# Kernel optimization log

Measured on AMD Instinct MI355X. Metric: run time of the kernel, lower is better.

The kernel has to match this reference:

```python
import jax, jax.numpy as jnp
import numpy as np

N_NODES = 100000


def _add_self_loops(edge_index, n):
    loop = jnp.arange(n, dtype=edge_index.dtype)
    src = jnp.concatenate([edge_index[0], loop])
    dst = jnp.concatenate([edge_index[1], loop])
    return src, dst


def _gcn_conv(x, W, b, src, dst, n):
    # h = X W, then symmetric-normalized scatter-add over edges (PyG GCNConv)
    h = x @ W
    ones = jnp.ones(src.shape[0], dtype=h.dtype)
    deg = jax.ops.segment_sum(ones, dst, num_segments=n)  # in-degree incl. self loops
    dinv = jnp.where(deg > 0, jax.lax.rsqrt(deg), 0.0)
    norm = dinv[src] * dinv[dst]                           # [E]
    msg = h[src] * norm[:, None]                           # gather + scale
    out = jax.ops.segment_sum(msg, dst, num_segments=n)    # scatter-add
    return out + b


def setup_inputs() -> dict:
    key = jax.random.key(0)
    k1, k2, k3, k4 = jax.random.split(key, 4)
    F, H, C = 128, 128, 16
    x = jax.random.normal(k1, (N_NODES, F), dtype=jnp.float32)
    edge_index = jax.random.randint(k2, (2, 1600000), 0, N_NODES, dtype=jnp.int64)
    W1 = jax.random.normal(k3, (F, H), dtype=jnp.float32) / np.sqrt(F)
    b1 = jnp.zeros((H,), dtype=jnp.float32)
    W2 = jax.random.normal(k4, (H, C), dtype=jnp.float32) / np.sqrt(H)
    b2 = jnp.zeros((C,), dtype=jnp.float32)
    return {"x": x, "edge_index": edge_index, "W1": W1, "b1": b1, "W2": W2, "b2": b2}


def reference(x, edge_index, W1, b1, W2, b2):
    n = x.shape[0]
    src, dst = _add_self_loops(edge_index, n)
    h = _gcn_conv(x, W1, b1, src, dst, n)
    h = jax.nn.relu(h)
    # dropout(p=0.1) treated as identity (deterministic eval-mode reference)
    logits = _gcn_conv(h, W2, b2, src, dst, n)
    return logits, jax.nn.log_softmax(logits, axis=1)
```

## Files before the change

kernel.cpp:

```cpp
#include <hip/hip_runtime.h>
#include <math.h>


#define ELLW 72
#define EPB 16384
#define BSH 9
#define MAXEB 100
#define MAXBK 200

typedef __attribute__((ext_vector_type(8))) short short8;
typedef __attribute__((ext_vector_type(4))) float f32x4;
typedef __attribute__((ext_vector_type(4))) int i32x4;
typedef __attribute__((ext_vector_type(4))) _Float16 f16x4;

__device__ __forceinline__ float bf2f(unsigned short u) {
    return __uint_as_float(((unsigned int)u) << 16);
}
__device__ __forceinline__ unsigned short f2bf(float f) {
    unsigned int u = __float_as_uint(f);
    unsigned int r = (u + 0x7fffu + ((u >> 16) & 1u)) >> 16;
    return (unsigned short)r;
}
__device__ __forceinline__ f32x4 h2f4(f16x4 v) {
    f32x4 r;
    r[0] = (float)v[0]; r[1] = (float)v[1]; r[2] = (float)v[2]; r[3] = (float)v[3];
    return r;
}

__global__ void k_prep_hist(unsigned short* __restrict__ h, _Float16* __restrict__ g,
                            const float* __restrict__ W1, unsigned short* __restrict__ wt,
                            int n, const int* __restrict__ dst, int E,
                            int* __restrict__ hist, int nbuck, float* __restrict__ dinv) {
    __shared__ int lh[MAXBK];
    const int t = threadIdx.x;
    if (blockIdx.x < 64) {
        int i = blockIdx.x * 256 + t;
        if (i < 16384) {
            int nc = i >> 7, k = i & 127;
            wt[i] = f2bf(W1[k * 128 + nc]);
        }
        if (i < 128) h[(size_t)n * 128 + i] = 0;
        if (i < 16) g[(size_t)n * 16 + i] = (_Float16)0.f;
        if (i < 1) dinv[n] = 1.f;
        return;
    }
    const int blk = blockIdx.x - 64;
    for (int i = t; i < nbuck; i += 256) lh[i] = 0;
    __syncthreads();
    const int e0 = blk * EPB;
    const int e1 = min(e0 + EPB, E);
    for (int e = e0 + t; e < e1; e += 256)
        atomicAdd(&lh[dst[e] >> BSH], 1);
    __syncthreads();
    for (int i = t; i < nbuck; i += 256)
        hist[blk * nbuck + i] = lh[i];
}

__global__ void k_scan(int* __restrict__ hist, int* __restrict__ bstart,
                       int* __restrict__ bcount, int neb, int nbuck) {
    __shared__ unsigned short lh[MAXEB * MAXBK];
    __shared__ int sc[256];
    const int t = threadIdx.x;
    const int items = neb * nbuck;
    const int it4 = items >> 2;
    for (int i = t; i < it4; i += 256) {
        i32x4 v = *(const i32x4*)(hist + i * 4);
        lh[i * 4 + 0] = (unsigned short)v[0];
        lh[i * 4 + 1] = (unsigned short)v[1];
        lh[i * 4 + 2] = (unsigned short)v[2];
        lh[i * 4 + 3] = (unsigned short)v[3];
    }
    for (int i = (it4 << 2) + t; i < items; i += 256)
        lh[i] = (unsigned short)hist[i];
    __syncthreads();
    int total = 0;
    if (t < nbuck)
        for (int blk = 0; blk < neb; ++blk) total += lh[blk * nbuck + t];
    sc[t] = total;
    __syncthreads();
    for (int o = 1; o < 256; o <<= 1) {
        int x = 0;
        if (t >= o) x = sc[t - o];
        __syncthreads();
        if (t >= o) sc[t] += x;
        __syncthreads();
    }
    if (t < nbuck) {
        int run = sc[t] - total;
        bstart[t] = run;
        bcount[t] = total;
        for (int blk = 0; blk < neb; ++blk) {
            int idx = blk * nbuck + t;
            int v = lh[idx];
            hist[idx] = run;
            run += v;
        }
    }
}

__global__ __launch_bounds__(256) void k_bin_gemm(
        const int* __restrict__ src, const int* __restrict__ dst, int E,
        const int* __restrict__ hist, int* __restrict__ binned, int nbuck, int neb,
        const float* __restrict__ x, const unsigned short* __restrict__ wt,
        unsigned short* __restrict__ h, int n) {
    __shared__ unsigned short xs[64 * 136];
    const int t = threadIdx.x;
    if ((int)blockIdx.x < neb) {
        int* cnt = (int*)xs;
        const int blk = blockIdx.x;
        for (int i = t; i < nbuck; i += 256) cnt[i] = hist[blk * nbuck + i];
        __syncthreads();
        const int e0 = blk * EPB;
        const int e1 = min(e0 + EPB, E);
        for (int e = e0 + t; e < e1; e += 256) {
            int d = dst[e];
            int b = d >> BSH;
            int pos = atomicAdd(&cnt[b], 1);
            binned[pos] = src[e] | ((d & ((1 << BSH) - 1)) << 17);
        }
        return;
    }
    const int row0 = ((int)blockIdx.x - neb) * 64;
    for (int i = t; i < 2048; i += 256) {
        int r = i >> 5, c4 = (i & 31) << 2;
        int gr = row0 + r;
        float4 v = make_float4(0.f, 0.f, 0.f, 0.f);
        if (gr < n) v = *(const float4*)(x + (size_t)gr * 128 + c4);
        ushort4 u;
        u.x = f2bf(v.x); u.y = f2bf(v.y); u.z = f2bf(v.z); u.w = f2bf(v.w);
        *(ushort4*)(xs + r * 136 + c4) = u;
    }
    __syncthreads();
    const int w = t >> 6;
    const int lane = t & 63;
    const int m = lane & 15, q = lane >> 4;
    f32x4 acc[8];
#pragma unroll
    for (int ns = 0; ns < 8; ++ns) acc[ns] = (f32x4){0.f, 0.f, 0.f, 0.f};
#pragma unroll
    for (int kt = 0; kt < 4; ++kt) {
        short8 a = *(const short8*)(xs + (w * 16 + m) * 136 + kt * 32 + q * 8);
#pragma unroll
        for (int ns = 0; ns < 8; ++ns) {
            short8 b = *(const short8*)((const short*)wt + (ns * 16 + m) * 128 + kt * 32 + q * 8);
            acc[ns] = __builtin_amdgcn_mfma_f32_16x16x32_bf16(a, b, acc[ns], 0, 0, 0);
        }
    }
    unsigned short* xsw = xs + (w * 16) * 136;
#pragma unroll
    for (int ns = 0; ns < 8; ++ns)
#pragma unroll
        for (int reg = 0; reg < 4; ++reg)
            xsw[(q * 4 + reg) * 136 + ns * 16 + m] = f2bf(acc[ns][reg]);
    __syncthreads();
#pragma unroll
    for (int it = 0; it < 8; ++it) {
        int rl = (lane >> 5) + it * 2;
        int off = (lane & 31) * 4;
        int gr = row0 + w * 16 + rl;
        if (gr < n)
            *(ushort4*)(h + (size_t)gr * 128 + off) = *(const ushort4*)(xsw + rl * 136 + off);
    }
}

__global__ void k_ell(const int* __restrict__ binned, const int* __restrict__ bstart,
                      const int* __restrict__ bcount, int* __restrict__ deg,
                      float* __restrict__ dinv, int* __restrict__ col, int n) {
    __shared__ int ldeg[1 << BSH];
    const int t = threadIdx.x, b = blockIdx.x;
    const int node0 = b << BSH;
    for (int i = t; i < (1 << BSH); i += 256) ldeg[i] = 0;
    __syncthreads();
    const int st = bstart[b], cv = bcount[b];
    for (int i = t; i < cv; i += 256) {
        int v = binned[st + i];
        int s = v & 0x1FFFF;
        int dl = v >> 17;
        int q = atomicAdd(&ldeg[dl], 1);
        if (q < ELLW) col[(size_t)(node0 + dl) * ELLW + q] = s;
    }
    __syncthreads();
    for (int i = t; i < (1 << BSH); i += 256) {
        int node = node0 + i;
        if (node < n) {
            int dgv = ldeg[i];
            deg[node] = dgv;
            int dc = dgv > ELLW ? ELLW : dgv;
            dinv[node] = rsqrtf((float)(dc + 1));
            int kend = (dc + 7) & ~7;
            for (int q = dc; q < kend; ++q) col[(size_t)node * ELLW + q] = n;
        }
    }
}

__global__ __launch_bounds__(256, 2) void k_gather1f(
        const unsigned short* __restrict__ h, const int* __restrict__ deg,
        const float* __restrict__ dinv, const int* __restrict__ col,
        const float* __restrict__ b1, const float* __restrict__ W2,
        _Float16* __restrict__ g, int n) {
    const int t = threadIdx.x;
    const int lane = t & 15;
    const int d = blockIdx.x * 16 + (t >> 4);
    if (d >= n) return;
    int dg = deg[d];
    if (dg > ELLW) dg = ELLW;
    const float dd = dinv[d];
    const int kend = (dg + 7) & ~7;
    const int* ecol = col + (size_t)d * ELLW;

    float aA[8], aB[8];
    {
        short8 u = *(const short8*)(h + (size_t)d * 128 + lane * 8);
#pragma unroll
        for (int j = 0; j < 8; ++j) {
            aA[j] = dd * bf2f((unsigned short)u[j]);
            aB[j] = 0.f;
        }
    }
    for (int k = 0; k < kend; k += 8) {
        int4 c0 = *(const int4*)(ecol + k);
        int4 c1 = *(const int4*)(ecol + k + 4);
        float e0 = dinv[c0.x], e1 = dinv[c0.y], e2 = dinv[c0.z], e3 = dinv[c0.w];
        float e4 = dinv[c1.x], e5 = dinv[c1.y], e6 = dinv[c1.z], e7 = dinv[c1.w];
        short8 u0 = *(const short8*)(h + (size_t)c0.x * 128 + lane * 8);
        short8 u1 = *(const short8*)(h + (size_t)c0.y * 128 + lane * 8);
        short8 u2 = *(const short8*)(h + (size_t)c0.z * 128 + lane * 8);
        short8 u3 = *(const short8*)(h + (size_t)c0.w * 128 + lane * 8);
        short8 u4 = *(const short8*)(h + (size_t)c1.x * 128 + lane * 8);
        short8 u5 = *(const short8*)(h + (size_t)c1.y * 128 + lane * 8);
        short8 u6 = *(const short8*)(h + (size_t)c1.z * 128 + lane * 8);
        short8 u7 = *(const short8*)(h + (size_t)c1.w * 128 + lane * 8);
#pragma unroll
        for (int j = 0; j < 8; ++j) {
            aA[j] = fmaf(bf2f((unsigned short)u0[j]), e0, aA[j]);
            aB[j] = fmaf(bf2f((unsigned short)u1[j]), e1, aB[j]);
            aA[j] = fmaf(bf2f((unsigned short)u2[j]), e2, aA[j]);
            aB[j] = fmaf(bf2f((unsigned short)u3[j]), e3, aB[j]);
            aA[j] = fmaf(bf2f((unsigned short)u4[j]), e4, aA[j]);
            aB[j] = fmaf(bf2f((unsigned short)u5[j]), e5, aB[j]);
            aA[j] = fmaf(bf2f((unsigned short)u6[j]), e6, aA[j]);
            aB[j] = fmaf(bf2f((unsigned short)u7[j]), e7, aB[j]);
        }
    }
    float y[8];
    const float* b1p = b1 + lane * 8;
#pragma unroll
    for (int j = 0; j < 8; ++j)
        y[j] = fmaxf(fmaf(aA[j] + aB[j], dd, b1p[j]), 0.f);
    const float4* w2v = (const float4*)(W2 + lane * 8 * 16);
    float4 z0 = make_float4(0.f, 0.f, 0.f, 0.f);
    float4 z1 = z0, z2 = z0, z3 = z0;
#pragma unroll
    for (int j = 0; j < 8; ++j) {
        float4 w0 = w2v[j * 4 + 0], w1 = w2v[j * 4 + 1];
        float4 w2 = w2v[j * 4 + 2], w3 = w2v[j * 4 + 3];
        float yj = y[j];
        z0.x = fmaf(yj, w0.x, z0.x); z0.y = fmaf(yj, w0.y, z0.y);
        z0.z = fmaf(yj, w0.z, z0.z); z0.w = fmaf(yj, w0.w, z0.w);
        z1.x = fmaf(yj, w1.x, z1.x); z1.y = fmaf(yj, w1.y, z1.y);
        z1.z = fmaf(yj, w1.z, z1.z); z1.w = fmaf(yj, w1.w, z1.w);
        z2.x = fmaf(yj, w2.x, z2.x); z2.y = fmaf(yj, w2.y, z2.y);
        z2.z = fmaf(yj, w2.z, z2.z); z2.w = fmaf(yj, w2.w, z2.w);
        z3.x = fmaf(yj, w3.x, z3.x); z3.y = fmaf(yj, w3.y, z3.y);
        z3.z = fmaf(yj, w3.z, z3.z); z3.w = fmaf(yj, w3.w, z3.w);
    }
#pragma unroll
    for (int mm = 1; mm < 16; mm <<= 1) {
        z0.x += __shfl_xor(z0.x, mm); z0.y += __shfl_xor(z0.y, mm);
        z0.z += __shfl_xor(z0.z, mm); z0.w += __shfl_xor(z0.w, mm);
        z1.x += __shfl_xor(z1.x, mm); z1.y += __shfl_xor(z1.y, mm);
        z1.z += __shfl_xor(z1.z, mm); z1.w += __shfl_xor(z1.w, mm);
        z2.x += __shfl_xor(z2.x, mm); z2.y += __shfl_xor(z2.y, mm);
        z2.z += __shfl_xor(z2.z, mm); z2.w += __shfl_xor(z2.w, mm);
        z3.x += __shfl_xor(z3.x, mm); z3.y += __shfl_xor(z3.y, mm);
        z3.z += __shfl_xor(z3.z, mm); z3.w += __shfl_xor(z3.w, mm);
    }
    if (lane < 4) {
        float4 z = (lane == 0) ? z0 : (lane == 1) ? z1 : (lane == 2) ? z2 : z3;
        f16x4 zz;
        zz[0] = (_Float16)(z.x * dd); zz[1] = (_Float16)(z.y * dd);
        zz[2] = (_Float16)(z.z * dd); zz[3] = (_Float16)(z.w * dd);
        *(f16x4*)(g + (size_t)d * 16 + lane * 4) = zz;
    }
}

__global__ void k_gather2(const _Float16* __restrict__ g, const int* __restrict__ deg,
                          const int* __restrict__ col, const float* __restrict__ b2,
                          float* __restrict__ out, int n) {
    const int t = threadIdx.x;
    const int d = blockIdx.x * 64 + (t >> 2);
    if (d >= n) return;
    const int l = t & 3;
    int dg = deg[d];
    if (dg > ELLW) dg = ELLW;
    const float dd = rsqrtf((float)(dg + 1));
    const int kend = (dg + 7) & ~7;
    const int* ecol = col + (size_t)d * ELLW;
    const _Float16* gl = g + l * 4;

    f32x4 aA = h2f4(*(const f16x4*)(gl + (size_t)d * 16));
    f32x4 aB = (f32x4){0.f, 0.f, 0.f, 0.f};
    f32x4 aC = aB, aD = aB;
    for (int k = 0; k < kend; k += 8) {
        int4 c0 = *(const int4*)(ecol + k);
        int4 c1 = *(const int4*)(ecol + k + 4);
        f16x4 h0 = *(const f16x4*)(gl + (size_t)c0.x * 16);
        f16x4 h1 = *(const f16x4*)(gl + (size_t)c0.y * 16);
        f16x4 h2 = *(const f16x4*)(gl + (size_t)c0.z * 16);
        f16x4 h3 = *(const f16x4*)(gl + (size_t)c0.w * 16);
        f16x4 h4 = *(const f16x4*)(gl + (size_t)c1.x * 16);
        f16x4 h5 = *(const f16x4*)(gl + (size_t)c1.y * 16);
        f16x4 h6 = *(const f16x4*)(gl + (size_t)c1.z * 16);
        f16x4 h7 = *(const f16x4*)(gl + (size_t)c1.w * 16);
        aA += h2f4(h0); aB += h2f4(h1); aC += h2f4(h2); aD += h2f4(h3);
        aA += h2f4(h4); aB += h2f4(h5); aC += h2f4(h6); aD += h2f4(h7);
    }
    f32x4 bv = *(const f32x4*)(b2 + l * 4);
    f32x4 acc = (aA + aB + aC + aD) * dd + bv;
    *(f32x4*)(out + (size_t)d * 16 + l * 4) = acc;
    float m = fmaxf(fmaxf(acc[0], acc[1]), fmaxf(acc[2], acc[3]));
    m = fmaxf(m, __shfl_xor(m, 1));
    m = fmaxf(m, __shfl_xor(m, 2));
    float e = expf(acc[0] - m) + expf(acc[1] - m) + expf(acc[2] - m) + expf(acc[3] - m);
    e += __shfl_xor(e, 1);
    e += __shfl_xor(e, 2);
    float ls = m + logf(e);
    f32x4 o;
    o[0] = acc[0] - ls; o[1] = acc[1] - ls; o[2] = acc[2] - ls; o[3] = acc[3] - ls;
    *(f32x4*)(out + (size_t)n * 16 + (size_t)d * 16 + l * 4) = o;
}

static inline size_t align256(size_t v) { return (v + 255) & ~(size_t)255; }

extern "C" void kernel_launch(void* const* d_in, const int* in_sizes, int n_in,
                              void* d_out, int out_size, void* d_ws, size_t ws_size,
                              hipStream_t stream) {
    const float* x  = (const float*)d_in[0];
    const int*   ei = (const int*)d_in[1];
    const float* W1 = (const float*)d_in[2];
    const float* b1 = (const float*)d_in[3];
    const float* W2 = (const float*)d_in[4];
    const float* b2 = (const float*)d_in[5];
    float* out = (float*)d_out;

    const int n = in_sizes[0] / 128;
    const int E = in_sizes[1] / 2;
    const int* src = ei;
    const int* dst = ei + E;
    const int NEB = (E + EPB - 1) / EPB;
    const int NBUCK = (n + (1 << BSH) - 1) >> BSH;

    char* base = (char*)d_ws;
    size_t off = 0;
    int* deg = (int*)(base + off); off = align256(off + (size_t)n * 4);
    float* dinv = (float*)(base + off); off = align256(off + ((size_t)n + 1) * 4);
    int* col = (int*)(base + off); off = align256(off + (size_t)n * ELLW * 4);
    unsigned short* wt = (unsigned short*)(base + off); off = align256(off + 128 * 128 * 2);
    unsigned short* h = (unsigned short*)(base + off); off = align256(off + ((size_t)n + 1) * 128 * 2);
    _Float16* g = (_Float16*)(base + off); off = align256(off + ((size_t)n + 1) * 16 * 2);
    int* hist = (int*)(base + off); off = align256(off + (size_t)MAXEB * MAXBK * 4);
    int* bstart = (int*)(base + off); off = align256(off + (size_t)MAXBK * 4);
    int* bcount = (int*)(base + off); off = align256(off + (size_t)MAXBK * 4);
    int* binned = (int*)(base + off); off = align256(off + (size_t)E * 4);

    k_prep_hist<<<64 + NEB, 256, 0, stream>>>(h, g, W1, wt, n, dst, E, hist, NBUCK, dinv);
    k_scan<<<1, 256, 0, stream>>>(hist, bstart, bcount, NEB, NBUCK);
    k_bin_gemm<<<NEB + (n + 63) / 64, 256, 0, stream>>>(
        src, dst, E, hist, binned, NBUCK, NEB, x, wt, h, n);
    k_ell<<<NBUCK, 256, 0, stream>>>(binned, bstart, bcount, deg, dinv, col, n);

    k_gather1f<<<(n + 15) / 16, 256, 0, stream>>>(h, deg, dinv, col, b1, W2, g, n);

    k_gather2<<<(n + 63) / 64, 256, 0, stream>>>(g, deg, col, b2, out, n);
}
```

Baseline: 347.7 us.

## Stage ELL column build in shared memory via counting sort for coalesced writes

The ELL builder first counts per-node degrees, prefix-sums the capped counts, and scatters edge sources into a shared-memory buffer sorted by destination. It then writes each node's full ELLW-wide row with coalesced 16-byte stores, padding the unused slots. This replaces scattered 4-byte global writes with contiguous ones. The cost is a second pass over the binned input, an extra shared scan, more shared memory per block, and writing full 72-wide rows instead of only the padded-to-8 part. Blocks with more edges than the buffer holds fall back to the old path.

```diff
diff --git a/kernel.cpp b/kernel.cpp
--- a/kernel.cpp
+++ b/kernel.cpp
@@ -7,6 +7,7 @@
 #define BSH 9
 #define MAXEB 100
 #define MAXBK 200
+#define SORTCAP 10240
 
 typedef __attribute__((ext_vector_type(8))) short short8;
 typedef __attribute__((ext_vector_type(4))) float f32x4;
@@ -163,32 +164,85 @@
     }
 }
 
-__global__ void k_ell(const int* __restrict__ binned, const int* __restrict__ bstart,
-                      const int* __restrict__ bcount, int* __restrict__ deg,
-                      float* __restrict__ dinv, int* __restrict__ col, int n) {
+__global__ __launch_bounds__(256) void k_ell(
+        const int* __restrict__ binned, const int* __restrict__ bstart,
+        const int* __restrict__ bcount, int* __restrict__ deg,
+        float* __restrict__ dinv, int* __restrict__ col, int n) {
+    __shared__ int sorted[SORTCAP];
     __shared__ int ldeg[1 << BSH];
+    __shared__ int off[1 << BSH];
+    __shared__ int cur[1 << BSH];
+    __shared__ int psum[256];
     const int t = threadIdx.x, b = blockIdx.x;
     const int node0 = b << BSH;
-    for (int i = t; i < (1 << BSH); i += 256) ldeg[i] = 0;
-    __syncthreads();
     const int st = bstart[b], cv = bcount[b];
-    for (int i = t; i < cv; i += 256) {
-        int v = binned[st + i];
-        int s = v & 0x1FFFF;
-        int dl = v >> 17;
-        int q = atomicAdd(&ldeg[dl], 1);
-        if (q < ELLW) col[(size_t)(node0 + dl) * ELLW + q] = s;
-    }
-    __syncthreads();
+    for (int i = t; i < (1 << BSH); i += 256) { ldeg[i] = 0; cur[i] = 0; }
+    __syncthreads();
+    for (int i = t; i < cv; i += 256)
+        atomicAdd(&ldeg[binned[st + i] >> 17], 1);
+    __syncthreads();
+
+    if (cv <= SORTCAP) {
+        int c0 = min(ldeg[2 * t], ELLW);
+        int c1 = min(ldeg[2 * t + 1], ELLW);
+        psum[t] = c0 + c1;
+        __syncthreads();
+        for (int o = 1; o < 256; o <<= 1) {
+            int v = 0;
+            if (t >= o) v = psum[t - o];
+            __syncthreads();
+            psum[t] += v;
+            __syncthreads();
+        }
+        int base = psum[t] - (c0 + c1);
+        off[2 * t] = base;
+        off[2 * t + 1] = base + c0;
+        __syncthreads();
+        for (int i = t; i < cv; i += 256) {
+            int v = binned[st + i];
+            int dl = v >> 17;
+            int r = atomicAdd(&cur[dl], 1);
+            if (r < ELLW) sorted[off[dl] + r] = v & 0x1FFFF;
+        }
+        __syncthreads();
+        const int nn = min(1 << BSH, n - node0);
+        const int totv = nn * (ELLW / 4);
+        int* colb = col + (size_t)node0 * ELLW;
+        for (int idx = t; idx < totv; idx += 256) {
+            int i = idx / (ELLW / 4);
+            int q = (idx - i * (ELLW / 4)) * 4;
+            int dc = min(ldeg[i], ELLW);
+            int o = off[i];
+            i32x4 v;
+#pragma unroll
+            for (int j = 0; j < 4; ++j)
+                v[j] = (q + j < dc) ? sorted[o + q + j] : n;
+            *(i32x4*)(colb + (size_t)i * ELLW + q) = v;
+        }
+    } else {
+        for (int i = t; i < cv; i += 256) {
+            int v = binned[st + i];
+            int s = v & 0x1FFFF;
+            int dl = v >> 17;
+            int r = atomicAdd(&cur[dl], 1);
+            if (r < ELLW) col[(size_t)(node0 + dl) * ELLW + r] = s;
+        }
+        __syncthreads();
+        for (int i = t; i < (1 << BSH); i += 256) {
+            int node = node0 + i;
+            if (node < n) {
+                int dc = min(ldeg[i], ELLW);
+                int kend = (dc + 7) & ~7;
+                for (int q = dc; q < kend; ++q) col[(size_t)node * ELLW + q] = n;
+            }
+        }
+    }
     for (int i = t; i < (1 << BSH); i += 256) {
         int node = node0 + i;
         if (node < n) {
             int dgv = ldeg[i];
             deg[node] = dgv;
-            int dc = dgv > ELLW ? ELLW : dgv;
-            dinv[node] = rsqrtf((float)(dc + 1));
-            int kend = (dc + 7) & ~7;
-            for (int q = dc; q < kend; ++q) col[(size_t)node * ELLW + q] = n;
+            dinv[node] = rsqrtf((float)(min(dgv, ELLW) + 1));
         }
     }
 }
```

Result: no change. 344.1 us (-1.0%).
